# Kernel optimization log

Measured on AMD Instinct MI355X. Metric: run time of the kernel, lower is better.

## Reference

```python
import jax, jax.numpy as jnp
import numpy as np


def _mlp2(x, w1, b1, w2, b2):
    # Linear -> LeakyReLU(0.01, torch default) -> Linear
    return jax.nn.leaky_relu(x @ w1 + b1) @ w2 + b2


def _fuse(vis, phr):
    # pairwise fusion: concat[vis, phr, vis*phr, vis-phr] -> last dim 4*R
    shp = jnp.broadcast_shapes(vis.shape, phr.shape)
    v = jnp.broadcast_to(vis, shp)
    p = jnp.broadcast_to(phr, shp)
    return jnp.concatenate([v, p, v * p, v - p], axis=-1)


def setup_inputs() -> dict:
    key = jax.random.key(0)
    B, P, N, D, R = 4, 16, 256, 2048, 1024
    ks = jax.random.split(key, 16)
    w = lambda k, s: jax.random.normal(k, s, jnp.float32) * 0.02
    inp = {
        "box_feats": jax.random.normal(ks[0], (B, N, D), jnp.float32),
        "phrase_embed": jax.random.normal(ks[1], (B, P, R), jnp.float32),
        # visual_embedding MLP (stage 1)
        "ve_w1": w(ks[2], (D, R)), "ve_b1": jnp.zeros((R,), jnp.float32),
        "ve_w2": w(ks[3], (R, R)), "ve_b2": jnp.zeros((R,), jnp.float32),
        # similarity MLP: 4R -> 256 -> 1
        "sim_w1": w(ks[4], (4 * R, 256)), "sim_b1": jnp.zeros((256,), jnp.float32),
        "sim_w2": w(ks[5], (256, 1)), "sim_b2": jnp.zeros((1,), jnp.float32),
        # box_reg MLP: 4R -> 256 -> 4
        "reg_w1": w(ks[6], (4 * R, 256)), "reg_b1": jnp.zeros((256,), jnp.float32),
        "reg_w2": w(ks[7], (256, 4)), "reg_b2": jnp.zeros((4,), jnp.float32),
        # topN-stage twins
        "vet_w1": w(ks[8], (D, R)), "vet_b1": jnp.zeros((R,), jnp.float32),
        "vet_w2": w(ks[9], (R, R)), "vet_b2": jnp.zeros((R,), jnp.float32),
        "simt_w1": w(ks[10], (4 * R, 256)), "simt_b1": jnp.zeros((256,), jnp.float32),
        "simt_w2": w(ks[11], (256, 1)), "simt_b2": jnp.zeros((1,), jnp.float32),
        "regt_w1": w(ks[12], (4 * R, 256)), "regt_b1": jnp.zeros((256,), jnp.float32),
        "regt_w2": w(ks[13], (256, 4)), "regt_b2": jnp.zeros((4,), jnp.float32),
        "topN": 16,
    }
    return inp


def reference(box_feats, phrase_embed,
              ve_w1, ve_b1, ve_w2, ve_b2,
              sim_w1, sim_b1, sim_w2, sim_b2,
              reg_w1, reg_b1, reg_w2, reg_b2,
              vet_w1, vet_b1, vet_w2, vet_b2,
              simt_w1, simt_b1, simt_w2, simt_b2,
              regt_w1, regt_b1, regt_w2, regt_b2,
              topN):
    # Stage 1: embed all boxes, score every (phrase, box) pair.
    vis = _mlp2(box_feats, ve_w1, ve_b1, ve_w2, ve_b2)          # [B,N,R]
    fused = _fuse(vis[:, None], phrase_embed[:, :, None])        # [B,P,N,4R]
    sim = jax.nn.softmax(
        _mlp2(fused, sim_w1, sim_b1, sim_w2, sim_b2)[..., 0], axis=-1)  # [B,P,N]
    reg = _mlp2(fused, reg_w1, reg_b1, reg_w2, reg_b2)           # [B,P,N,4]

    # Stage 2: topN rescoring per phrase (make_pair_topN pattern).
    _, top_idx = jax.lax.top_k(sim, topN)                        # [B,P,topN]
    bf_top = jnp.take_along_axis(box_feats[:, None], top_idx[..., None], axis=2)  # [B,P,topN,D]
    vis_t = _mlp2(bf_top, vet_w1, vet_b1, vet_w2, vet_b2)        # [B,P,topN,R]
    fused_t = _fuse(vis_t, phrase_embed[:, :, None])             # [B,P,topN,4R]
    sim_t = jax.nn.softmax(
        _mlp2(fused_t, simt_w1, simt_b1, simt_w2, simt_b2)[..., 0], axis=-1)  # [B,P,topN]
    reg_t = _mlp2(fused_t, regt_w1, regt_b1, regt_w2, regt_b2)   # [B,P,topN,4]
    return (sim, reg, sim_t, reg_t)
```

## Files before the change

kernel.cpp:

```cpp
#include <hip/hip_runtime.h>
#include <hip/hip_bf16.h>


namespace {

constexpr int Nc_   = 256;
constexpr int Dc    = 2048;
constexpr int Rc    = 1024;
constexpr int TOPN  = 16;
constexpr int NCAND = 32;
constexpr int HS    = 256;
constexpr int HO    = 512;
constexpr int BPc   = 64;
constexpr int PAIRS1 = 16384;
constexpr int PAIRS2 = 1024;
constexpr int CPAIRS = BPc * NCAND;

__device__ __forceinline__ float  leaky01f(float x)  { return x > 0.f ? x : 0.01f * x; }
__device__ __forceinline__ double leaky01d(double x) { return x > 0.0 ? x : 0.01  * x; }

template <typename TA, typename TW, bool LEAKY>
__global__ __launch_bounds__(256) void dg64_kernel(
    const TA* __restrict__ A, const TW* __restrict__ W, const float* __restrict__ bias,
    double* __restrict__ C64, int M, int N, int K)
{
  __shared__ double As[16][33];
  __shared__ double Bs[16][66];
  const int t = threadIdx.x, tx = t & 15, ty = t >> 4;
  const int row0 = blockIdx.y * 32, col0 = blockIdx.x * 64;
  double acc[2][4] = {};

  const int mm = t >> 3, kqa = (t & 7) * 2;
  const int kkb = t >> 4, nqb = (t & 15) * 4;

  for (int k0 = 0; k0 < K; k0 += 16) {
    {
      const TA* src = A + (size_t)(row0 + mm) * K + k0 + kqa;
      double v0, v1;
      if constexpr (sizeof(TA) == 4) {
        float2 f = *(const float2*)src; v0 = f.x; v1 = f.y;
      } else {
        double2 d = *(const double2*)src; v0 = d.x; v1 = d.y;
      }
      As[kqa][mm] = v0; As[kqa + 1][mm] = v1;
    }
    {
      const TW* src = W + (size_t)(k0 + kkb) * N + col0 + nqb;
      if constexpr (sizeof(TW) == 4) {
        float4 f = *(const float4*)src;
        Bs[kkb][nqb] = f.x; Bs[kkb][nqb + 1] = f.y;
        Bs[kkb][nqb + 2] = f.z; Bs[kkb][nqb + 3] = f.w;
      } else {
        double2 a = *(const double2*)src, b = *(const double2*)(src + 2);
        Bs[kkb][nqb] = a.x; Bs[kkb][nqb + 1] = a.y;
        Bs[kkb][nqb + 2] = b.x; Bs[kkb][nqb + 3] = b.y;
      }
    }
    __syncthreads();
#pragma unroll
    for (int kk = 0; kk < 16; ++kk) {
      double a[2], b[4];
#pragma unroll
      for (int i = 0; i < 2; ++i) a[i] = As[kk][ty * 2 + i];
#pragma unroll
      for (int j = 0; j < 4; ++j) b[j] = Bs[kk][tx + 16 * j];
#pragma unroll
      for (int i = 0; i < 2; ++i)
#pragma unroll
        for (int j = 0; j < 4; ++j) acc[i][j] = fma(a[i], b[j], acc[i][j]);
    }
    __syncthreads();
  }

#pragma unroll
  for (int i = 0; i < 2; ++i) {
    int r = row0 + ty * 2 + i;
#pragma unroll
    for (int j = 0; j < 4; ++j) {
      int c = col0 + tx + 16 * j;
      double v = acc[i][j];
      if (bias) v += (double)bias[c];
      if constexpr (LEAKY) v = leaky01d(v);
      C64[(size_t)r * N + c] = v;
    }
  }
}

__global__ __launch_bounds__(256) void pair64c_kernel(
    const double* __restrict__ vis, const float* __restrict__ phr,
    const double* __restrict__ W, const double* __restrict__ Xv,
    const double* __restrict__ Xp, const double* __restrict__ b1,
    const int* __restrict__ candn, double* __restrict__ H)
{
  __shared__ double As[16][33];
  __shared__ double Bs[16][66];
  const int t = threadIdx.x, tx = t & 15, ty = t >> 4;
  const int row0 = blockIdx.y * 32, col0 = blockIdx.x * 64;
  double acc[2][4] = {};

  const int mm = t >> 3, kqa = (t & 7) * 2;
  const int kkb = t >> 4, nqb = (t & 15) * 4;
  const int ms = row0 + mm, bps = ms >> 5;
  const int vrs = ((bps >> 4) << 8) | candn[ms], prs = bps;

  for (int k0 = 0; k0 < Rc; k0 += 16) {
    {
      double2 v = *(const double2*)(vis + (size_t)vrs * Rc + k0 + kqa);
      float2  p = *(const float2*)(phr + (size_t)prs * Rc + k0 + kqa);
      As[kqa][mm]     = v.x * (double)p.x;
      As[kqa + 1][mm] = v.y * (double)p.y;
    }
    {
      const double* src = W + (size_t)(k0 + kkb) * HS + col0 + nqb;
      double2 a = *(const double2*)src, b = *(const double2*)(src + 2);
      Bs[kkb][nqb] = a.x; Bs[kkb][nqb + 1] = a.y;
      Bs[kkb][nqb + 2] = b.x; Bs[kkb][nqb + 3] = b.y;
    }
    __syncthreads();
#pragma unroll
    for (int kk = 0; kk < 16; ++kk) {
      double a[2], b[4];
#pragma unroll
      for (int i = 0; i < 2; ++i) a[i] = As[kk][ty * 2 + i];
#pragma unroll
      for (int j = 0; j < 4; ++j) b[j] = Bs[kk][tx + 16 * j];
#pragma unroll
      for (int i = 0; i < 2; ++i)
#pragma unroll
        for (int j = 0; j < 4; ++j) acc[i][j] = fma(a[i], b[j], acc[i][j]);
    }
    __syncthreads();
  }

#pragma unroll
  for (int i = 0; i < 2; ++i) {
    int r = row0 + ty * 2 + i, bp = r >> 5;
    int vr = ((bp >> 4) << 8) | candn[r], pr = bp;
#pragma unroll
    for (int j = 0; j < 4; ++j) {
      int c = col0 + tx + 16 * j;
      double v = acc[i][j] + Xv[(size_t)vr * HS + c] + Xp[(size_t)pr * HS + c] + b1[c];
      H[(size_t)r * HS + c] = leaky01d(v);
    }
  }
}

template <int BM, int BN, int BK, int TM, int TN>
__global__ __launch_bounds__(256) void sgemm_kernel(
    const float* __restrict__ A, const float* __restrict__ W,
    const float* __restrict__ bias, float* __restrict__ C,
    int M, int Nc, int K, int leaky)
{
  constexpr int THREADS = (BM / TM) * (BN / TN);
  static_assert(THREADS == 256, "block must be 256");
  __shared__ float As[BK][BM];
  __shared__ float Bs[BK][BN];

  const int t = threadIdx.x;
  const int tx = t % (BN / TN), ty = t / (BN / TN);
  const int row0 = blockIdx.y * BM, col0 = blockIdx.x * BN;
  float acc[TM][TN] = {};

  for (int k0 = 0; k0 < K; k0 += BK) {
    constexpr int AV = BM * BK / 4 / THREADS;
#pragma unroll
    for (int p_ = 0; p_ < AV; ++p_) {
      int f = p_ * THREADS + t;
      int mm = f / (BK / 4), kq = (f % (BK / 4)) * 4;
      float4 a4 = *(const float4*)(A + (size_t)(row0 + mm) * K + k0 + kq);
      As[kq + 0][mm] = a4.x; As[kq + 1][mm] = a4.y;
      As[kq + 2][mm] = a4.z; As[kq + 3][mm] = a4.w;
    }
    constexpr int BV = BK * BN / 4 / THREADS;
#pragma unroll
    for (int p_ = 0; p_ < BV; ++p_) {
      int f = p_ * THREADS + t;
      int nq = (f % (BN / 4)) * 4, kk = f / (BN / 4);
      *(float4*)&Bs[kk][nq] = *(const float4*)(W + (size_t)(k0 + kk) * Nc + col0 + nq);
    }
    __syncthreads();
#pragma unroll
    for (int kk = 0; kk < BK; ++kk) {
      float a[TM], bb[TN];
#pragma unroll
      for (int i = 0; i < TM; i += 4) {
        float4 v = *(const float4*)&As[kk][ty * TM + i];
        a[i] = v.x; a[i + 1] = v.y; a[i + 2] = v.z; a[i + 3] = v.w;
      }
#pragma unroll
      for (int j = 0; j < TN; j += 4) {
        float4 v = *(const float4*)&Bs[kk][tx * TN + j];
        bb[j] = v.x; bb[j + 1] = v.y; bb[j + 2] = v.z; bb[j + 3] = v.w;
      }
#pragma unroll
      for (int i = 0; i < TM; ++i)
#pragma unroll
        for (int j = 0; j < TN; ++j) acc[i][j] = fmaf(a[i], bb[j], acc[i][j]);
    }
    __syncthreads();
  }

#pragma unroll
  for (int i = 0; i < TM; ++i) {
    int r = row0 + ty * TM + i;
#pragma unroll
    for (int j = 0; j < TN; j += 4) {
      int c = col0 + tx * TN + j;
      float4 o;
      o.x = acc[i][j]; o.y = acc[i][j + 1]; o.z = acc[i][j + 2]; o.w = acc[i][j + 3];
      if (bias) {
        float4 bv = *(const float4*)(bias + c);
        o.x += bv.x; o.y += bv.y; o.z += bv.z; o.w += bv.w;
      }
      if (leaky) { o.x = leaky01f(o.x); o.y = leaky01f(o.y); o.z = leaky01f(o.z); o.w = leaky01f(o.w); }
      *(float4*)(C + (size_t)r * Nc + c) = o;
    }
  }
}

template <int BM, int BN, int BK, int TM, int TN, int STAGE, int NCOL>
__global__ __launch_bounds__(256) void pair_gemm_kernel(
    const float* __restrict__ vis, const float* __restrict__ phr,
    const float* __restrict__ Wvp, const float* __restrict__ Xv,
    const float* __restrict__ Xp, const float* __restrict__ b1c,
    float* __restrict__ Hout, int M)
{
  constexpr int THREADS = (BM / TM) * (BN / TN);
  static_assert(THREADS == 256, "block must be 256");
  __shared__ float As[BK][BM];
  __shared__ float Bs[BK][BN];

  const int t = threadIdx.x;
  const int tx = t % (BN / TN), ty = t / (BN / TN);
  const int row0 = blockIdx.y * BM, col0 = blockIdx.x * BN;
  float acc[TM][TN] = {};

  for (int k0 = 0; k0 < Rc; k0 += BK) {
    constexpr int AV = BM * BK / 4 / THREADS;
#pragma unroll
    for (int p_ = 0; p_ < AV; ++p_) {
      int f = p_ * THREADS + t;
      int mm = f / (BK / 4), kq = (f % (BK / 4)) * 4;
      int m = row0 + mm;
      int vr, pr;
      if (STAGE == 1) { int bp = m >> 8; pr = bp; vr = ((bp >> 4) << 8) | (m & 255); }
      else            { vr = m; pr = m >> 4; }
      float4 v4 = *(const float4*)(vis + (size_t)vr * Rc + k0 + kq);
      float4 p4 = *(const float4*)(phr + (size_t)pr * Rc + k0 + kq);
      As[kq + 0][mm] = v4.x * p4.x; As[kq + 1][mm] = v4.y * p4.y;
      As[kq + 2][mm] = v4.z * p4.z; As[kq + 3][mm] = v4.w * p4.w;
    }
    constexpr int BV = BK * BN / 4 / THREADS;
#pragma unroll
    for (int p_ = 0; p_ < BV; ++p_) {
      int f = p_ * THREADS + t;
      int nq = (f % (BN / 4)) * 4, kk = f / (BN / 4);
      *(float4*)&Bs[kk][nq] = *(const float4*)(Wvp + (size_t)(k0 + kk) * NCOL + col0 + nq);
    }
    __syncthreads();
#pragma unroll
    for (int kk = 0; kk < BK; ++kk) {
      float a[TM], bb[TN];
#pragma unroll
      for (int i = 0; i < TM; i += 4) {
        float4 v = *(const float4*)&As[kk][ty * TM + i];
        a[i] = v.x; a[i + 1] = v.y; a[i + 2] = v.z; a[i + 3] = v.w;
      }
#pragma unroll
      for (int j = 0; j < TN; j += 4) {
        float4 v = *(const float4*)&Bs[kk][tx * TN + j];
        bb[j] = v.x; bb[j + 1] = v.y; bb[j + 2] = v.z; bb[j + 3] = v.w;
      }
#pragma unroll
      for (int i = 0; i < TM; ++i)
#pragma unroll
        for (int j = 0; j < TN; ++j) acc[i][j] = fmaf(a[i], bb[j], acc[i][j]);
    }
    __syncthreads();
  }

#pragma unroll
  for (int i = 0; i < TM; ++i) {
    int r = row0 + ty * TM + i;
    int vr, pr;
    if (STAGE == 1) { int bp = r >> 8; pr = bp; vr = ((bp >> 4) << 8) | (r & 255); }
    else            { vr = r; pr = r >> 4; }
#pragma unroll
    for (int j = 0; j < TN; j += 4) {
      int c = col0 + tx * TN + j;
      float4 xv = *(const float4*)(Xv + (size_t)vr * NCOL + c);
      float4 xp = *(const float4*)(Xp + (size_t)pr * NCOL + c);
      float4 bv = *(const float4*)(b1c + c);
      float4 o;
      o.x = leaky01f(acc[i][j]     + xv.x + xp.x + bv.x);
      o.y = leaky01f(acc[i][j + 1] + xv.y + xp.y + bv.y);
      o.z = leaky01f(acc[i][j + 2] + xv.z + xp.z + bv.z);
      o.w = leaky01f(acc[i][j + 3] + xv.w + xp.w + bv.w);
      *(float4*)(Hout + (size_t)r * NCOL + c) = o;
    }
  }
}

__global__ __launch_bounds__(256) void prep_stage1_kernel(
    const float* __restrict__ sim_w1, const float* __restrict__ sim_b1,
    const float* __restrict__ reg_w1, const float* __restrict__ reg_b1,
    double* __restrict__ WV64, double* __restrict__ WP64, double* __restrict__ WVP64,
    double* __restrict__ b64,
    float* __restrict__ W1V, float* __restrict__ W1P, float* __restrict__ W1VP,
    float* __restrict__ b1)
{
  int bid = blockIdx.x;
  if (bid < 1024) {
    int idx = bid * 256 + threadIdx.x;
    int r = idx >> 8, c = idx & 255;
    double wa = (double)sim_w1[(size_t)(0 * Rc + r) * 256 + c];
    double wb = (double)sim_w1[(size_t)(1 * Rc + r) * 256 + c];
    double wc = (double)sim_w1[(size_t)(2 * Rc + r) * 256 + c];
    double wd = (double)sim_w1[(size_t)(3 * Rc + r) * 256 + c];
    WV64[idx] = wa + wd; WP64[idx] = wb - wd; WVP64[idx] = wc;
    if (r == 0) b64[c] = (double)sim_b1[c];
  } else {
    int idx = (bid - 1024) * 256 + threadIdx.x;
    int r = idx >> 9, j = idx & (HO - 1);
    const float* w1 = (j < 256) ? sim_w1 : reg_w1;
    int c = j & 255;
    float wa = w1[(size_t)(0 * Rc + r) * 256 + c];
    float wb = w1[(size_t)(1 * Rc + r) * 256 + c];
    float wc = w1[(size_t)(2 * Rc + r) * 256 + c];
    float wd = w1[(size_t)(3 * Rc + r) * 256 + c];
    W1V[idx] = wa + wd; W1P[idx] = wb - wd; W1VP[idx] = wc;
    if (r == 0) b1[j] = (j < 256) ? sim_b1[c] : reg_b1[c];
  }
}

__global__ __launch_bounds__(256) void prep_t_kernel(
    const float* __restrict__ simw1, const float* __restrict__ regw1,
    const float* __restrict__ simb1, const float* __restrict__ regb1,
    float* __restrict__ Wv, float* __restrict__ Wp, float* __restrict__ Wvp,
    float* __restrict__ b1c)
{
  int idx = blockIdx.x * 256 + threadIdx.x;
  int r = idx >> 9, j = idx & (HO - 1);
  const float* w1 = (j < 256) ? simw1 : regw1;
  int c = j & 255;
  float wa = w1[(size_t)(0 * Rc + r) * 256 + c];
  float wb = w1[(size_t)(1 * Rc + r) * 256 + c];
  float wc = w1[(size_t)(2 * Rc + r) * 256 + c];
  float wd = w1[(size_t)(3 * Rc + r) * 256 + c];
  Wv[idx] = wa + wd; Wp[idx] = wb - wd; Wvp[idx] = wc;
  if (r == 0) b1c[j] = (j < 256) ? simb1[c] : regb1[c];
}

__global__ __launch_bounds__(256) void layer2_t_kernel(
    const float* __restrict__ hidden,
    const float* __restrict__ sw2, const float* __restrict__ sb2,
    const float* __restrict__ rw2, const float* __restrict__ rb2,
    float* __restrict__ sim_logits, float* __restrict__ reg_out, int M)
{
  int wave = (blockIdx.x * blockDim.x + threadIdx.x) >> 6, lane = threadIdx.x & 63;
  if (wave >= M) return;
  const float* h = hidden + (size_t)wave * HO;
  float4 hs = *(const float4*)(h + lane * 4);
  float4 hr = *(const float4*)(h + 256 + lane * 4);
  float4 ws = *(const float4*)(sw2 + lane * 4);
  float s = hs.x * ws.x + hs.y * ws.y + hs.z * ws.z + hs.w * ws.w;
  float4 r0 = *(const float4*)(rw2 + (size_t)(lane * 4 + 0) * 4);
  float4 r1 = *(const float4*)(rw2 + (size_t)(lane * 4 + 1) * 4);
  float4 r2 = *(const float4*)(rw2 + (size_t)(lane * 4 + 2) * 4);
  float4 r3 = *(const float4*)(rw2 + (size_t)(lane * 4 + 3) * 4);
  float c0 = hr.x * r0.x + hr.y * r1.x + hr.z * r2.x + hr.w * r3.x;
  float c1 = hr.x * r0.y + hr.y * r1.y + hr.z * r2.y + hr.w * r3.y;
  float c2 = hr.x * r0.z + hr.y * r1.z + hr.z * r2.z + hr.w * r3.z;
  float c3 = hr.x * r0.w + hr.y * r1.w + hr.z * r2.w + hr.w * r3.w;
#pragma unroll
  for (int off = 32; off; off >>= 1) {
    s  += __shfl_xor(s, off);
    c0 += __shfl_xor(c0, off); c1 += __shfl_xor(c1, off);
    c2 += __shfl_xor(c2, off); c3 += __shfl_xor(c3, off);
  }
  if (lane == 0) {
    sim_logits[wave] = s + sb2[0];
    float4 o; o.x = c0 + rb2[0]; o.y = c1 + rb2[1]; o.z = c2 + rb2[2]; o.w = c3 + rb2[3];
    *(float4*)(reg_out + (size_t)wave * 4) = o;
  }
}

__global__ __launch_bounds__(256) void layer2_sim64_kernel(
    const double* __restrict__ h, const float* __restrict__ sw2,
    const float* __restrict__ sb2, double* __restrict__ out, int M)
{
  int wave = (blockIdx.x * blockDim.x + threadIdx.x) >> 6, lane = threadIdx.x & 63;
  if (wave >= M) return;
  const double* hr = h + (size_t)wave * HS + lane * 4;
  double2 h0 = *(const double2*)hr, h1 = *(const double2*)(hr + 2);
  float4 w = *(const float4*)(sw2 + lane * 4);
  double s = h0.x * (double)w.x + h0.y * (double)w.y + h1.x * (double)w.z + h1.y * (double)w.w;
#pragma unroll
  for (int off = 32; off; off >>= 1) s += __shfl_xor(s, off);
  if (lane == 0) out[wave] = s + (double)sb2[0];
}

__global__ __launch_bounds__(64) void softmax_cand32_kernel(
    const float* __restrict__ logits, float* __restrict__ sim_out,
    int* __restrict__ candn)
{
  int row = blockIdx.x, lane = threadIdx.x;
  float v[4];
#pragma unroll
  for (int i = 0; i < 4; ++i) v[i] = logits[row * 256 + i * 64 + lane];
  float m = fmaxf(fmaxf(v[0], v[1]), fmaxf(v[2], v[3]));
#pragma unroll
  for (int off = 32; off; off >>= 1) m = fmaxf(m, __shfl_xor(m, off));
  float e[4], ssum = 0.f;
#pragma unroll
  for (int i = 0; i < 4; ++i) { e[i] = expf(v[i] - m); ssum += e[i]; }
#pragma unroll
  for (int off = 32; off; off >>= 1) ssum += __shfl_xor(ssum, off);
#pragma unroll
  for (int i = 0; i < 4; ++i)
    sim_out[row * 256 + i * 64 + lane] = e[i] / ssum;
  for (int it = 0; it < NCAND; ++it) {
    float bv = -3.0e38f; int bi = 0;
#pragma unroll
    for (int i = 0; i < 4; ++i)
      if (v[i] > bv) { bv = v[i]; bi = i * 64 + lane; }
#pragma unroll
    for (int off = 32; off; off >>= 1) {
      float ov = __shfl_xor(bv, off);
      int   oi = __shfl_xor(bi, off);
      if (ov > bv || (ov == bv && oi < bi)) { bv = ov; bi = oi; }
    }
    if (lane == 0) candn[row * NCAND + it] = bi;
    if ((bi & 63) == lane) v[bi >> 6] = -3.4e38f;
  }
}

__global__ __launch_bounds__(64) void topk_cand64_kernel(
    const double* __restrict__ clog, const int* __restrict__ candn,
    int* __restrict__ top_idx)
{
  int row = blockIdx.x, lane = threadIdx.x;
  double v = (lane < NCAND) ? clog[row * NCAND + lane] : -1.0e300;
  int    n = (lane < NCAND) ? candn[row * NCAND + lane] : (1 << 29);
  const double EPS = 2.5e-7;
  for (int it = 0; it < TOPN; ++it) {
    double vm = v;
#pragma unroll
    for (int off = 32; off; off >>= 1) vm = fmax(vm, __shfl_xor(vm, off));
    double thr = vm - EPS;
    int bn = (v >= thr) ? n : (1 << 30);
#pragma unroll
    for (int off = 32; off; off >>= 1) {
      int o = __shfl_xor(bn, off);
      if (o < bn) bn = o;
    }
    if (lane == 0) top_idx[row * TOPN + it] = bn;
    if (n == bn) v = -1.0e300;
  }
}

__global__ __launch_bounds__(64) void softmax16_kernel(
    const float* __restrict__ logits, float* __restrict__ out)
{
  int row = blockIdx.x, lane = threadIdx.x;
  float v = (lane < TOPN) ? logits[row * TOPN + lane] : -1e30f;
  float m = v;
#pragma unroll
  for (int off = 8; off; off >>= 1) m = fmaxf(m, __shfl_xor(m, off));
  float e = (lane < TOPN) ? expf(v - m) : 0.f;
  float s = e;
#pragma unroll
  for (int off = 8; off; off >>= 1) s += __shfl_xor(s, off);
  if (lane < TOPN) out[row * TOPN + lane] = e / s;
}

__global__ __launch_bounds__(256) void gather_kernel(
    const float* __restrict__ box, const int* __restrict__ top_idx,
    float* __restrict__ bf_top)
{
  int pr = blockIdx.x;
  int bp = pr >> 4, b = bp >> 4;
  int src = b * Nc_ + top_idx[pr];
  const float4* s = (const float4*)(box + (size_t)src * Dc);
  float4* d = (float4*)(bf_top + (size_t)pr * Dc);
  for (int i = threadIdx.x; i < Dc / 4; i += 256) d[i] = s[i];
}

}

extern "C" void kernel_launch(void* const* d_in, const int* in_sizes, int n_in,
                              void* d_out, int out_size, void* d_ws, size_t ws_size,
                              hipStream_t stream) {
  const float* box    = (const float*)d_in[0];
  const float* phrase = (const float*)d_in[1];
  const float* ve_w1  = (const float*)d_in[2];
  const float* ve_b1  = (const float*)d_in[3];
  const float* ve_w2  = (const float*)d_in[4];
  const float* ve_b2  = (const float*)d_in[5];
  const float* sim_w1 = (const float*)d_in[6];
  const float* sim_b1 = (const float*)d_in[7];
  const float* sim_w2 = (const float*)d_in[8];
  const float* sim_b2 = (const float*)d_in[9];
  const float* reg_w1 = (const float*)d_in[10];
  const float* reg_b1 = (const float*)d_in[11];
  const float* reg_w2 = (const float*)d_in[12];
  const float* reg_b2 = (const float*)d_in[13];
  const float* vet_w1 = (const float*)d_in[14];
  const float* vet_b1 = (const float*)d_in[15];
  const float* vet_w2 = (const float*)d_in[16];
  const float* vet_b2 = (const float*)d_in[17];
  const float* simt_w1 = (const float*)d_in[18];
  const float* simt_b1 = (const float*)d_in[19];
  const float* simt_w2 = (const float*)d_in[20];
  const float* simt_b2 = (const float*)d_in[21];
  const float* regt_w1 = (const float*)d_in[22];
  const float* regt_b1 = (const float*)d_in[23];
  const float* regt_w2 = (const float*)d_in[24];
  const float* regt_b2 = (const float*)d_in[25];

  float* out = (float*)d_out;
  float* o_sim  = out;
  float* o_reg  = out + PAIRS1;
  float* o_simt = out + 81920;
  float* o_regt = out + 82944;

  constexpr size_t MB = 1u << 20;
  char* w = (char*)d_ws;
  double* WcV64  = (double*)(w + 0 * MB);
  double* WcP64  = (double*)(w + 2 * MB);
  double* WcVP64 = (double*)(w + 4 * MB);
  float*  Wc1V   = (float*)(w + 6 * MB);
  float*  Wc1P   = (float*)(w + 8 * MB);
  float*  Wc1VP  = (float*)(w + 10 * MB);
  char* sm = w + 12 * MB;
  double* b1c64    = (double*)(sm + 0);
  float*  b1c1     = (float*) (sm + 4096);
  float*  b1ct     = (float*) (sm + 8192);
  int*    candn    = (int*)   (sm + 12288);
  double* clog64   = (double*)(sm + 24576);
  int*    topidx   = (int*)   (sm + 40960);
  float*  simtlog  = (float*) (sm + 45056);
  float*  simlog32 = (float*) (sm + 65536);
  float*  Xp32     = (float*) (sm + 131072);
  double* Xp64     = (double*)(sm + 262144);
  float*  Xpt      = (float*) (sm + 393216);
  float*  H1_32 = (float*)(w + 12 * MB + 524288);
  float*  Xv32  = (float*)(w + 12 * MB + 524288);
  float*  vis32 = (float*)(w + 16 * MB + 524288);
  double* vis64 = (double*)(w + 12 * MB + 524288);
  char* big = w + 20 * MB + 524288;
  float*  hid1  = (float*)(big);
  double* H64   = (double*)(big);
  double* Xv64  = (double*)(big + 8 * MB);
  double* H2    = (double*)(big + 10 * MB);
  float*  bftop = (float*)(big);
  float*  H1t   = (float*)(big + 8 * MB);
  float*  vist  = (float*)(big + 12 * MB);
  float*  Xvt   = (float*)(big + 16 * MB);
  float*  hidnt = (float*)(big + 18 * MB);
  float*  WcVt  = (float*)(big + 20 * MB);
  float*  WcPt  = (float*)(big + 22 * MB);
  float*  WcVPt = (float*)(big + 24 * MB);

  prep_stage1_kernel<<<3072, 256, 0, stream>>>(
      sim_w1, sim_b1, reg_w1, reg_b1,
      WcV64, WcP64, WcVP64, b1c64, Wc1V, Wc1P, Wc1VP, b1c1);
  sgemm_kernel<64, 64, 32, 4, 4><<<dim3(16, 16), 256, 0, stream>>>(
      box, ve_w1, ve_b1, H1_32, 1024, Rc, Dc, 1);
  sgemm_kernel<64, 64, 32, 4, 4><<<dim3(16, 16), 256, 0, stream>>>(
      H1_32, ve_w2, ve_b2, vis32, 1024, Rc, Rc, 0);
  sgemm_kernel<64, 64, 32, 4, 4><<<dim3(8, 16), 256, 0, stream>>>(
      vis32, Wc1V, nullptr, Xv32, 1024, HO, Rc, 0);
  sgemm_kernel<64, 64, 32, 4, 4><<<dim3(8, 1), 256, 0, stream>>>(
      phrase, Wc1P, nullptr, Xp32, BPc, HO, Rc, 0);
  pair_gemm_kernel<128, 128, 32, 8, 8, 1, HO><<<dim3(4, 128), 256, 0, stream>>>(
      vis32, phrase, Wc1VP, Xv32, Xp32, b1c1, hid1, PAIRS1);
  layer2_t_kernel<<<PAIRS1 / 4, 256, 0, stream>>>(
      hid1, sim_w2, sim_b2, reg_w2, reg_b2, simlog32, o_reg, PAIRS1);
  softmax_cand32_kernel<<<BPc, 64, 0, stream>>>(simlog32, o_sim, candn);

  dg64_kernel<float, float, true><<<dim3(16, 32), 256, 0, stream>>>(
      box, ve_w1, ve_b1, H64, 1024, Rc, Dc);
  dg64_kernel<double, float, false><<<dim3(16, 32), 256, 0, stream>>>(
      H64, ve_w2, ve_b2, vis64, 1024, Rc, Rc);
  dg64_kernel<double, double, false><<<dim3(4, 32), 256, 0, stream>>>(
      vis64, WcV64, nullptr, Xv64, 1024, HS, Rc);
  dg64_kernel<float, double, false><<<dim3(4, 2), 256, 0, stream>>>(
      phrase, WcP64, nullptr, Xp64, BPc, HS, Rc);
  pair64c_kernel<<<dim3(4, CPAIRS / 32), 256, 0, stream>>>(
      vis64, phrase, WcVP64, Xv64, Xp64, b1c64, candn, H2);
  layer2_sim64_kernel<<<CPAIRS / 4, 256, 0, stream>>>(
      H2, sim_w2, sim_b2, clog64, CPAIRS);
  topk_cand64_kernel<<<BPc, 64, 0, stream>>>(clog64, candn, topidx);

  prep_t_kernel<<<Rc * HO / 256, 256, 0, stream>>>(
      simt_w1, regt_w1, simt_b1, regt_b1, WcVt, WcPt, WcVPt, b1ct);
  gather_kernel<<<PAIRS2, 256, 0, stream>>>(box, topidx, bftop);
  sgemm_kernel<64, 64, 32, 4, 4><<<dim3(16, 16), 256, 0, stream>>>(
      bftop, vet_w1, vet_b1, H1t, 1024, Rc, Dc, 1);
  sgemm_kernel<64, 64, 32, 4, 4><<<dim3(16, 16), 256, 0, stream>>>(
      H1t, vet_w2, vet_b2, vist, 1024, Rc, Rc, 0);
  sgemm_kernel<64, 64, 32, 4, 4><<<dim3(8, 16), 256, 0, stream>>>(
      vist, WcVt, nullptr, Xvt, 1024, HO, Rc, 0);
  sgemm_kernel<64, 64, 32, 4, 4><<<dim3(8, 1), 256, 0, stream>>>(
      phrase, WcPt, nullptr, Xpt, BPc, HO, Rc, 0);
  pair_gemm_kernel<64, 64, 32, 4, 4, 2, HO><<<dim3(8, 16), 256, 0, stream>>>(
      vist, phrase, WcVPt, Xvt, Xpt, b1ct, hidnt, PAIRS2);
  layer2_t_kernel<<<PAIRS2 / 4, 256, 0, stream>>>(
      hidnt, simt_w2, simt_b2, regt_w2, regt_b2, simtlog, o_regt, PAIRS2);
  softmax16_kernel<<<BPc, 64, 0, stream>>>(simtlog, o_simt);
}
```

Baseline: 1.572 ms.

## Fuse layer-2 projections into stage-1 pair GEMM epilogue and swizzle LDS

The stage-1 pair GEMM now computes the second-layer sim and reg dot products in its epilogue. It reduces them with wave shuffles and atomically adds the partial sums into the logit and reg outputs, so the 16384x512 hidden tensor is never written or re-read. All weight-prep work and the zeroing of the atomic targets are merged into one launch. The A tile in LDS gets an XOR swizzle and the TN=8 B reads are split into two strided float4 loads to cut bank conflicts. The atomics make the summation order nondeterministic, which could slightly perturb the logits that feed the top-k selection.

```diff
diff --git a/kernel.cpp b/kernel.cpp
--- a/kernel.cpp
+++ b/kernel.cpp
@@ -19,6 +19,8 @@
 __device__ __forceinline__ float  leaky01f(float x)  { return x > 0.f ? x : 0.01f * x; }
 __device__ __forceinline__ double leaky01d(double x) { return x > 0.0 ? x : 0.01  * x; }
 
+__device__ __forceinline__ int aswz(int m, int k) { return m ^ (8 * ((k >> 2) & 7)); }
+
 template <typename TA, typename TW, bool LEAKY>
 __global__ __launch_bounds__(256) void dg64_kernel(
     const TA* __restrict__ A, const TW* __restrict__ W, const float* __restrict__ bias,
@@ -168,8 +170,9 @@
       int f = p_ * THREADS + t;
       int mm = f / (BK / 4), kq = (f % (BK / 4)) * 4;
       float4 a4 = *(const float4*)(A + (size_t)(row0 + mm) * K + k0 + kq);
-      As[kq + 0][mm] = a4.x; As[kq + 1][mm] = a4.y;
-      As[kq + 2][mm] = a4.z; As[kq + 3][mm] = a4.w;
+      int cs = aswz(mm, kq);
+      As[kq + 0][cs] = a4.x; As[kq + 1][cs] = a4.y;
+      As[kq + 2][cs] = a4.z; As[kq + 3][cs] = a4.w;
     }
     constexpr int BV = BK * BN / 4 / THREADS;
 #pragma unroll
@@ -182,9 +185,10 @@
 #pragma unroll
     for (int kk = 0; kk < BK; ++kk) {
       float a[TM], bb[TN];
+      int ab = aswz(ty * TM, kk);
 #pragma unroll
       for (int i = 0; i < TM; i += 4) {
-        float4 v = *(const float4*)&As[kk][ty * TM + i];
+        float4 v = *(const float4*)&As[kk][ab + i];
         a[i] = v.x; a[i + 1] = v.y; a[i + 2] = v.z; a[i + 3] = v.w;
       }
 #pragma unroll
@@ -218,12 +222,15 @@
   }
 }
 
-template <int BM, int BN, int BK, int TM, int TN, int STAGE, int NCOL>
+template <int BM, int BN, int BK, int TM, int TN, int STAGE, int NCOL, bool FUSE>
 __global__ __launch_bounds__(256) void pair_gemm_kernel(
     const float* __restrict__ vis, const float* __restrict__ phr,
     const float* __restrict__ Wvp, const float* __restrict__ Xv,
     const float* __restrict__ Xp, const float* __restrict__ b1c,
-    float* __restrict__ Hout, int M)
+    float* __restrict__ Hout,
+    const float* __restrict__ sw2, const float* __restrict__ sb2,
+    const float* __restrict__ rw2, const float* __restrict__ rb2,
+    float* __restrict__ simlog, float* __restrict__ rego)
 {
   constexpr int THREADS = (BM / TM) * (BN / TN);
   static_assert(THREADS == 256, "block must be 256");
@@ -247,8 +254,9 @@
       else            { vr = m; pr = m >> 4; }
       float4 v4 = *(const float4*)(vis + (size_t)vr * Rc + k0 + kq);
       float4 p4 = *(const float4*)(phr + (size_t)pr * Rc + k0 + kq);
-      As[kq + 0][mm] = v4.x * p4.x; As[kq + 1][mm] = v4.y * p4.y;
-      As[kq + 2][mm] = v4.z * p4.z; As[kq + 3][mm] = v4.w * p4.w;
+      int cs = aswz(mm, kq);
+      As[kq + 0][cs] = v4.x * p4.x; As[kq + 1][cs] = v4.y * p4.y;
+      As[kq + 2][cs] = v4.z * p4.z; As[kq + 3][cs] = v4.w * p4.w;
     }
     constexpr int BV = BK * BN / 4 / THREADS;
 #pragma unroll
@@ -261,15 +269,23 @@
 #pragma unroll
     for (int kk = 0; kk < BK; ++kk) {
       float a[TM], bb[TN];
+      int ab = aswz(ty * TM, kk);
 #pragma unroll
       for (int i = 0; i < TM; i += 4) {
-        float4 v = *(const float4*)&As[kk][ty * TM + i];
+        float4 v = *(const float4*)&As[kk][ab + i];
         a[i] = v.x; a[i + 1] = v.y; a[i + 2] = v.z; a[i + 3] = v.w;
       }
-#pragma unroll
-      for (int j = 0; j < TN; j += 4) {
-        float4 v = *(const float4*)&Bs[kk][tx * TN + j];
-        bb[j] = v.x; bb[j + 1] = v.y; bb[j + 2] = v.z; bb[j + 3] = v.w;
+      if constexpr (TN == 8) {
+        float4 v0 = *(const float4*)&Bs[kk][tx * 4];
+        float4 v1 = *(const float4*)&Bs[kk][64 + tx * 4];
+        bb[0] = v0.x; bb[1] = v0.y; bb[2] = v0.z; bb[3] = v0.w;
+        bb[4] = v1.x; bb[5] = v1.y; bb[6] = v1.z; bb[7] = v1.w;
+      } else {
+#pragma unroll
+        for (int j = 0; j < TN; j += 4) {
+          float4 v = *(const float4*)&Bs[kk][tx * TN + j];
+          bb[j] = v.x; bb[j + 1] = v.y; bb[j + 2] = v.z; bb[j + 3] = v.w;
+        }
       }
 #pragma unroll
       for (int i = 0; i < TM; ++i)
@@ -277,6 +293,25 @@
         for (int j = 0; j < TN; ++j) acc[i][j] = fmaf(a[i], bb[j], acc[i][j]);
     }
     __syncthreads();
+  }
+
+  const int cA = col0 + tx * 4;
+  const int cB = col0 + 64 + tx * 4;
+
+  float4 wsA, wsB;
+  float4 rwA[4], rwB[4];
+  bool is_sim = false;
+  if constexpr (FUSE) {
+    is_sim = (col0 < 256);
+    if (is_sim) {
+      wsA = *(const float4*)(sw2 + cA);
+      wsB = *(const float4*)(sw2 + cB);
+    } else {
+#pragma unroll
+      for (int j = 0; j < 4; ++j) rwA[j] = *(const float4*)(rw2 + (size_t)(cA + j - 256) * 4);
+#pragma unroll
+      for (int j = 0; j < 4; ++j) rwB[j] = *(const float4*)(rw2 + (size_t)(cB + j - 256) * 4);
+    }
   }
 
 #pragma unroll
@@ -285,29 +320,92 @@
     int vr, pr;
     if (STAGE == 1) { int bp = r >> 8; pr = bp; vr = ((bp >> 4) << 8) | (r & 255); }
     else            { vr = r; pr = r >> 4; }
-#pragma unroll
-    for (int j = 0; j < TN; j += 4) {
-      int c = col0 + tx * TN + j;
-      float4 xv = *(const float4*)(Xv + (size_t)vr * NCOL + c);
-      float4 xp = *(const float4*)(Xp + (size_t)pr * NCOL + c);
-      float4 bv = *(const float4*)(b1c + c);
-      float4 o;
-      o.x = leaky01f(acc[i][j]     + xv.x + xp.x + bv.x);
-      o.y = leaky01f(acc[i][j + 1] + xv.y + xp.y + bv.y);
-      o.z = leaky01f(acc[i][j + 2] + xv.z + xp.z + bv.z);
-      o.w = leaky01f(acc[i][j + 3] + xv.w + xp.w + bv.w);
-      *(float4*)(Hout + (size_t)r * NCOL + c) = o;
-    }
-  }
-}
-
-__global__ __launch_bounds__(256) void prep_stage1_kernel(
+    if constexpr (TN == 8) {
+      float h[8];
+      {
+        float4 xv = *(const float4*)(Xv + (size_t)vr * NCOL + cA);
+        float4 xp = *(const float4*)(Xp + (size_t)pr * NCOL + cA);
+        float4 bv = *(const float4*)(b1c + cA);
+        h[0] = leaky01f(acc[i][0] + xv.x + xp.x + bv.x);
+        h[1] = leaky01f(acc[i][1] + xv.y + xp.y + bv.y);
+        h[2] = leaky01f(acc[i][2] + xv.z + xp.z + bv.z);
+        h[3] = leaky01f(acc[i][3] + xv.w + xp.w + bv.w);
+      }
+      {
+        float4 xv = *(const float4*)(Xv + (size_t)vr * NCOL + cB);
+        float4 xp = *(const float4*)(Xp + (size_t)pr * NCOL + cB);
+        float4 bv = *(const float4*)(b1c + cB);
+        h[4] = leaky01f(acc[i][4] + xv.x + xp.x + bv.x);
+        h[5] = leaky01f(acc[i][5] + xv.y + xp.y + bv.y);
+        h[6] = leaky01f(acc[i][6] + xv.z + xp.z + bv.z);
+        h[7] = leaky01f(acc[i][7] + xv.w + xp.w + bv.w);
+      }
+      if constexpr (FUSE) {
+        if (is_sim) {
+          float part = h[0] * wsA.x + h[1] * wsA.y + h[2] * wsA.z + h[3] * wsA.w
+                     + h[4] * wsB.x + h[5] * wsB.y + h[6] * wsB.z + h[7] * wsB.w;
+#pragma unroll
+          for (int off = 8; off; off >>= 1) part += __shfl_xor(part, off);
+          if (tx == 0) {
+            if (col0 == 0) part += sb2[0];
+            atomicAdd(simlog + r, part);
+          }
+        } else {
+          float p0 = 0, p1 = 0, p2 = 0, p3 = 0;
+#pragma unroll
+          for (int j = 0; j < 4; ++j) {
+            p0 += h[j] * rwA[j].x; p1 += h[j] * rwA[j].y;
+            p2 += h[j] * rwA[j].z; p3 += h[j] * rwA[j].w;
+            p0 += h[j + 4] * rwB[j].x; p1 += h[j + 4] * rwB[j].y;
+            p2 += h[j + 4] * rwB[j].z; p3 += h[j + 4] * rwB[j].w;
+          }
+#pragma unroll
+          for (int off = 8; off; off >>= 1) {
+            p0 += __shfl_xor(p0, off); p1 += __shfl_xor(p1, off);
+            p2 += __shfl_xor(p2, off); p3 += __shfl_xor(p3, off);
+          }
+          if (tx == 0) {
+            if (col0 == 256) { p0 += rb2[0]; p1 += rb2[1]; p2 += rb2[2]; p3 += rb2[3]; }
+            atomicAdd(rego + (size_t)r * 4 + 0, p0);
+            atomicAdd(rego + (size_t)r * 4 + 1, p1);
+            atomicAdd(rego + (size_t)r * 4 + 2, p2);
+            atomicAdd(rego + (size_t)r * 4 + 3, p3);
+          }
+        }
+      } else {
+        *(float4*)(Hout + (size_t)r * NCOL + cA) = make_float4(h[0], h[1], h[2], h[3]);
+        *(float4*)(Hout + (size_t)r * NCOL + cB) = make_float4(h[4], h[5], h[6], h[7]);
+      }
+    } else {
+#pragma unroll
+      for (int j = 0; j < TN; j += 4) {
+        int c = col0 + tx * TN + j;
+        float4 xv = *(const float4*)(Xv + (size_t)vr * NCOL + c);
+        float4 xp = *(const float4*)(Xp + (size_t)pr * NCOL + c);
+        float4 bv = *(const float4*)(b1c + c);
+        float4 o;
+        o.x = leaky01f(acc[i][j]     + xv.x + xp.x + bv.x);
+        o.y = leaky01f(acc[i][j + 1] + xv.y + xp.y + bv.y);
+        o.z = leaky01f(acc[i][j + 2] + xv.z + xp.z + bv.z);
+        o.w = leaky01f(acc[i][j + 3] + xv.w + xp.w + bv.w);
+        *(float4*)(Hout + (size_t)r * NCOL + c) = o;
+      }
+    }
+  }
+}
+
+__global__ __launch_bounds__(256) void prep_all_kernel(
     const float* __restrict__ sim_w1, const float* __restrict__ sim_b1,
     const float* __restrict__ reg_w1, const float* __restrict__ reg_b1,
+    const float* __restrict__ simt_w1, const float* __restrict__ simt_b1,
+    const float* __restrict__ regt_w1, const float* __restrict__ regt_b1,
     double* __restrict__ WV64, double* __restrict__ WP64, double* __restrict__ WVP64,
     double* __restrict__ b64,
     float* __restrict__ W1V, float* __restrict__ W1P, float* __restrict__ W1VP,
-    float* __restrict__ b1)
+    float* __restrict__ b1,
+    float* __restrict__ WtV, float* __restrict__ WtP, float* __restrict__ WtVP,
+    float* __restrict__ bt,
+    float* __restrict__ zero_simlog, float* __restrict__ zero_rego)
 {
   int bid = blockIdx.x;
   if (bid < 1024) {
@@ -319,7 +417,7 @@
     double wd = (double)sim_w1[(size_t)(3 * Rc + r) * 256 + c];
     WV64[idx] = wa + wd; WP64[idx] = wb - wd; WVP64[idx] = wc;
     if (r == 0) b64[c] = (double)sim_b1[c];
-  } else {
+  } else if (bid < 3072) {
     int idx = (bid - 1024) * 256 + threadIdx.x;
     int r = idx >> 9, j = idx & (HO - 1);
     const float* w1 = (j < 256) ? sim_w1 : reg_w1;
@@ -330,25 +428,22 @@
     float wd = w1[(size_t)(3 * Rc + r) * 256 + c];
     W1V[idx] = wa + wd; W1P[idx] = wb - wd; W1VP[idx] = wc;
     if (r == 0) b1[j] = (j < 256) ? sim_b1[c] : reg_b1[c];
-  }
-}
-
-__global__ __launch_bounds__(256) void prep_t_kernel(
-    const float* __restrict__ simw1, const float* __restrict__ regw1,
-    const float* __restrict__ simb1, const float* __restrict__ regb1,
-    float* __restrict__ Wv, float* __restrict__ Wp, float* __restrict__ Wvp,
-    float* __restrict__ b1c)
-{
-  int idx = blockIdx.x * 256 + threadIdx.x;
-  int r = idx >> 9, j = idx & (HO - 1);
-  const float* w1 = (j < 256) ? simw1 : regw1;
-  int c = j & 255;
-  float wa = w1[(size_t)(0 * Rc + r) * 256 + c];
-  float wb = w1[(size_t)(1 * Rc + r) * 256 + c];
-  float wc = w1[(size_t)(2 * Rc + r) * 256 + c];
-  float wd = w1[(size_t)(3 * Rc + r) * 256 + c];
-  Wv[idx] = wa + wd; Wp[idx] = wb - wd; Wvp[idx] = wc;
-  if (r == 0) b1c[j] = (j < 256) ? simb1[c] : regb1[c];
+  } else if (bid < 5120) {
+    int idx = (bid - 3072) * 256 + threadIdx.x;
+    int r = idx >> 9, j = idx & (HO - 1);
+    const float* w1 = (j < 256) ? simt_w1 : regt_w1;
+    int c = j & 255;
+    float wa = w1[(size_t)(0 * Rc + r) * 256 + c];
+    float wb = w1[(size_t)(1 * Rc + r) * 256 + c];
+    float wc = w1[(size_t)(2 * Rc + r) * 256 + c];
+    float wd = w1[(size_t)(3 * Rc + r) * 256 + c];
+    WtV[idx] = wa + wd; WtP[idx] = wb - wd; WtVP[idx] = wc;
+    if (r == 0) bt[j] = (j < 256) ? simt_b1[c] : regt_b1[c];
+  } else if (bid < 5184) {
+    zero_simlog[(bid - 5120) * 256 + threadIdx.x] = 0.f;
+  } else {
+    zero_rego[(size_t)(bid - 5184) * 256 + threadIdx.x] = 0.f;
+  }
 }
 
 __global__ __launch_bounds__(256) void layer2_t_kernel(
@@ -545,12 +640,11 @@
   double* Xp64     = (double*)(sm + 262144);
   float*  Xpt      = (float*) (sm + 393216);
   float*  H1_32 = (float*)(w + 12 * MB + 524288);
-  float*  Xv32  = (float*)(w + 12 * MB + 524288);
   float*  vis32 = (float*)(w + 16 * MB + 524288);
   double* vis64 = (double*)(w + 12 * MB + 524288);
   char* big = w + 20 * MB + 524288;
-  float*  hid1  = (float*)(big);
   double* H64   = (double*)(big);
+  float*  Xv32  = (float*)(big + 8 * MB);
   double* Xv64  = (double*)(big + 8 * MB);
   double* H2    = (double*)(big + 10 * MB);
   float*  bftop = (float*)(big);
@@ -562,9 +656,10 @@
   float*  WcPt  = (float*)(big + 22 * MB);
   float*  WcVPt = (float*)(big + 24 * MB);
 
-  prep_stage1_kernel<<<3072, 256, 0, stream>>>(
-      sim_w1, sim_b1, reg_w1, reg_b1,
-      WcV64, WcP64, WcVP64, b1c64, Wc1V, Wc1P, Wc1VP, b1c1);
+  prep_all_kernel<<<5440, 256, 0, stream>>>(
+      sim_w1, sim_b1, reg_w1, reg_b1, simt_w1, simt_b1, regt_w1, regt_b1,
+      WcV64, WcP64, WcVP64, b1c64, Wc1V, Wc1P, Wc1VP, b1c1, WcVt, WcPt, WcVPt, b1ct,
+      simlog32, o_reg);
   sgemm_kernel<64, 64, 32, 4, 4><<<dim3(16, 16), 256, 0, stream>>>(
       box, ve_w1, ve_b1, H1_32, 1024, Rc, Dc, 1);
   sgemm_kernel<64, 64, 32, 4, 4><<<dim3(16, 16), 256, 0, stream>>>(
@@ -573,10 +668,9 @@
       vis32, Wc1V, nullptr, Xv32, 1024, HO, Rc, 0);
   sgemm_kernel<64, 64, 32, 4, 4><<<dim3(8, 1), 256, 0, stream>>>(
       phrase, Wc1P, nullptr, Xp32, BPc, HO, Rc, 0);
-  pair_gemm_kernel<128, 128, 32, 8, 8, 1, HO><<<dim3(4, 128), 256, 0, stream>>>(
-      vis32, phrase, Wc1VP, Xv32, Xp32, b1c1, hid1, PAIRS1);
-  layer2_t_kernel<<<PAIRS1 / 4, 256, 0, stream>>>(
-      hid1, sim_w2, sim_b2, reg_w2, reg_b2, simlog32, o_reg, PAIRS1);
+  pair_gemm_kernel<128, 128, 32, 8, 8, 1, HO, true><<<dim3(4, 128), 256, 0, stream>>>(
+      vis32, phrase, Wc1VP, Xv32, Xp32, b1c1, nullptr,
+      sim_w2, sim_b2, reg_w2, reg_b2, simlog32, o_reg);
   softmax_cand32_kernel<<<BPc, 64, 0, stream>>>(simlog32, o_sim, candn);
 
   dg64_kernel<float, float, true><<<dim3(16, 32), 256, 0, stream>>>(
@@ -593,8 +687,6 @@
       H2, sim_w2, sim_b2, clog64, CPAIRS);
   topk_cand64_kernel<<<BPc, 64, 0, stream>>>(clog64, candn, topidx);
 
-  prep_t_kernel<<<Rc * HO / 256, 256, 0, stream>>>(
-      simt_w1, regt_w1, simt_b1, regt_b1, WcVt, WcPt, WcVPt, b1ct);
   gather_kernel<<<PAIRS2, 256, 0, stream>>>(box, topidx, bftop);
   sgemm_kernel<64, 64, 32, 4, 4><<<dim3(16, 16), 256, 0, stream>>>(
       bftop, vet_w1, vet_b1, H1t, 1024, Rc, Dc, 1);
@@ -604,8 +696,9 @@
       vist, WcVt, nullptr, Xvt, 1024, HO, Rc, 0);
   sgemm_kernel<64, 64, 32, 4, 4><<<dim3(8, 1), 256, 0, stream>>>(
       phrase, WcPt, nullptr, Xpt, BPc, HO, Rc, 0);
-  pair_gemm_kernel<64, 64, 32, 4, 4, 2, HO><<<dim3(8, 16), 256, 0, stream>>>(
-      vist, phrase, WcVPt, Xvt, Xpt, b1ct, hidnt, PAIRS2);
+  pair_gemm_kernel<64, 64, 32, 4, 4, 2, HO, false><<<dim3(8, 16), 256, 0, stream>>>(
+      vist, phrase, WcVPt, Xvt, Xpt, b1ct, hidnt,
+      nullptr, nullptr, nullptr, nullptr, nullptr, nullptr);
   layer2_t_kernel<<<PAIRS2 / 4, 256, 0, stream>>>(
       hidnt, simt_w2, simt_b2, regt_w2, regt_b2, simtlog, o_regt, PAIRS2);
   softmax16_kernel<<<BPc, 64, 0, stream>>>(simtlog, o_simt);
```

Result: no change. 1.562 ms (-0.6%).
